# Performance work log

Measured on AMD Instinct MI355X. Metric: run time of the kernel, lower is better.

The kernel has to match this reference:

```python
import jax, jax.numpy as jnp
import numpy as np

LOG2 = 0.6931471805599453

def ssp(z):
    # SchNet shifted softplus
    return jax.nn.softplus(z) - jnp.asarray(LOG2, z.dtype)

def mlp(z, W1, b1, W2, b2):
    return ssp(z @ W1 + b1) @ W2 + b2

def _pair_idx(n_up, n_elec):
    # ordered electron pairs (i, j), i != j, grouped by spin of i and j
    n_down = n_elec - n_up
    up = np.arange(n_up)
    down = np.arange(n_up, n_elec)
    j_uu = np.stack([np.delete(up, i) for i in range(n_up)])            # [n_up, n_up-1]
    i_uu = np.repeat(up[:, None], max(n_up - 1, 0), axis=1)
    i_ud = np.repeat(up[:, None], n_down, axis=1)                        # [n_up, n_down]
    j_ud = np.broadcast_to(down, (n_up, n_down))
    i_du = np.repeat(down[:, None], n_up, axis=1)                        # [n_down, n_up]
    j_du = np.broadcast_to(up, (n_down, n_up))
    j_dd = np.stack([np.delete(down, i) for i in range(n_down)])         # [n_down, n_down-1]
    i_dd = np.repeat(down[:, None], max(n_down - 1, 0), axis=1)
    # label index: 0 = 'same', 1 = 'anti'
    return [(0, i_uu, j_uu), (1, i_ud, j_ud), (1, i_du, j_du), (0, i_dd, j_dd)]


def setup_inputs() -> dict:
    key = jax.random.key(0)
    ks = jax.random.split(key, 12)
    B, n_elec, n_nuc, dist, emb = 256, 64, 16, 32, 64
    s_in = 1.0 / np.sqrt(dist)
    s_emb = 1.0 / np.sqrt(emb)
    return {
        'x': jax.random.normal(ks[0], (B, n_elec, emb), jnp.float32),
        'Y': jax.random.normal(ks[1], (B, n_nuc, emb), jnp.float32),
        'edges_elec': jax.random.normal(ks[2], (B, n_elec, n_elec, dist), jnp.float32),
        'edges_nuc': jax.random.normal(ks[3], (B, n_elec, n_nuc, dist), jnp.float32),
        'w_W1': jax.random.normal(ks[4], (3, dist, emb), jnp.float32) * s_in,
        'w_b1': jnp.zeros((3, emb), jnp.float32),
        'w_W2': jax.random.normal(ks[5], (3, emb, emb), jnp.float32) * s_emb,
        'w_b2': jnp.zeros((3, emb), jnp.float32),
        'h_W1': jax.random.normal(ks[6], (emb, emb), jnp.float32) * s_emb,
        'h_b1': jnp.zeros((emb,), jnp.float32),
        'h_W2': jax.random.normal(ks[7], (emb, emb), jnp.float32) * s_emb,
        'h_b2': jnp.zeros((emb,), jnp.float32),
        'g_W1': jax.random.normal(ks[8], (3, emb, emb), jnp.float32) * s_emb,
        'g_b1': jnp.zeros((3, emb), jnp.float32),
        'g_W2': jax.random.normal(ks[9], (3, emb, emb), jnp.float32) * s_emb,
        'g_b2': jnp.zeros((3, emb), jnp.float32),
        'n_up': 32,
    }


def reference(x, Y, edges_elec, edges_nuc,
              w_W1, w_b1, w_W2, w_b2,
              h_W1, h_b1, h_W2, h_b2,
              g_W1, g_b1, g_W2, g_b2,
              n_up):
    n_elec = x.shape[-2]
    pairs = _pair_idx(int(n_up), n_elec)
    hx = mlp(x, h_W1, h_b1, h_W2, h_b2)  # shared h subnet, [..., n_elec, emb]
    # gather -> w subnet -> elementwise product with h(x)[j]
    msgs = [mlp(edges_elec[..., i, j, :], w_W1[l], w_b1[l], w_W2[l], w_b2[l]) * hx[..., j, :]
            for l, i, j in pairs]  # uu, ud, du, dd
    z_uu, z_ud, z_du, z_dd = (m.sum(axis=-2) for m in msgs)
    messages_el = jnp.concatenate([
        jnp.concatenate(msgs[:2], axis=-2),   # up rows: [.., n_up, n_elec-1, emb]
        jnp.concatenate(msgs[2:], axis=-2),   # down rows
    ], axis=-3)
    z_same = jnp.concatenate([z_uu, z_dd], axis=-2)
    z_anti = jnp.concatenate([z_ud, z_du], axis=-2)
    messages_nuc = mlp(edges_nuc, w_W1[2], w_b1[2], w_W2[2], w_b2[2]) * Y[..., None, :, :]
    z_nuc = messages_nuc.sum(axis=-2)
    # shared_g=False: separate g subnets (order: same, anti, n)
    update = (mlp(z_same, g_W1[0], g_b1[0], g_W2[0], g_b2[0])
              + mlp(z_anti, g_W1[1], g_b1[1], g_W2[1], g_b2[1])
              + mlp(z_nuc, g_W1[2], g_b1[2], g_W2[2], g_b2[2]))
    return update, messages_el, messages_nuc
```

## Files before the change

kernel.cpp:

```cpp
#include <hip/hip_runtime.h>
#include <hip/hip_bf16.h>

#define NE  64
#define NUP 32
#define NN  16
#define DD  32
#define EMB 64

__device__ __forceinline__ float ssp(float z) {
    float a = fabsf(z);
    float t = __expf(-a);
    return fmaxf(z, 0.0f) + __logf(1.0f + t) - 0.6931471805599453f;
}

__global__ __launch_bounds__(256) void k_hx(
    const float* __restrict__ x, const float* __restrict__ W1,
    const float* __restrict__ b1, const float* __restrict__ W2,
    const float* __restrict__ b2, float* __restrict__ hx)
{
    const int t = threadIdx.x;
    const int w = t >> 6;
    const int e = t & 63;
    const size_t row0 = (size_t)blockIdx.x * 4;

    __shared__ __align__(16) float sX[4][EMB];
    __shared__ float sh[4][EMB];

    if (t < 64) ((float4*)&sX[0][0])[t] = ((const float4*)(x + row0*EMB))[t];
    __syncthreads();

    float acc = b1[e];
    #pragma unroll
    for (int k = 0; k < EMB; ++k) acc = fmaf(sX[w][k], W1[k*EMB + e], acc);
    sh[w][e] = ssp(acc);
    __syncthreads();
    float acc2 = b2[e];
    #pragma unroll
    for (int k = 0; k < EMB; ++k) acc2 = fmaf(sh[w][k], W2[k*EMB + e], acc2);
    hx[(row0 + w)*EMB + e] = acc2;
}

__global__ __launch_bounds__(256, 3) void k_main(
    const float* __restrict__ eE,  const float* __restrict__ eN,
    const float* __restrict__ wW1, const float* __restrict__ wb1,
    const float* __restrict__ wW2, const float* __restrict__ wb2,
    const float* __restrict__ Y,   const float* __restrict__ hx,
    const float* __restrict__ gW1, const float* __restrict__ gb1,
    const float* __restrict__ gW2, const float* __restrict__ gb2,
    float* __restrict__ out_el, float* __restrict__ out_nuc, float* __restrict__ upd)
{
    const int blk = blockIdx.x;
    const int b = blk >> 6;
    const int i = blk & 63;
    const int t = threadIdx.x;
    const int w = t >> 6;
    const int e = t & 63;

    __shared__ __align__(16) float sE[NE][DD];
    __shared__ __align__(16) float sH1[NE][EMB];
    __shared__ __align__(16) float sHx[NE][EMB];
    __shared__ __align__(16) float sEN[NN][DD];
    __shared__ __align__(16) float sY[NN][EMB];
    __shared__ __align__(16) float sZp[4][EMB];
    __shared__ float sZS[EMB], sZA[EMB], sZN[EMB];
    __shared__ float sGH[3][EMB];
    __shared__ float sU[3][EMB];

    {
        const float4* eb4 = (const float4*)(eE + (size_t)blk * (NE*DD));
        float4* sE4 = (float4*)&sE[0][0];
        sE4[t]       = eb4[t];
        sE4[t + 256] = eb4[t + 256];
        const float4* hx4 = (const float4*)(hx + (size_t)b * (NE*EMB));
        float4* sHx4 = (float4*)&sHx[0][0];
        #pragma unroll
        for (int r = 0; r < 4; ++r) sHx4[t + 256*r] = hx4[t + 256*r];
        const float4* en4 = (const float4*)(eN + (size_t)blk * (NN*DD));
        if (t < 128) ((float4*)&sEN[0][0])[t] = en4[t];
        const float4* y4 = (const float4*)(Y + (size_t)b * (NN*EMB));
        ((float4*)&sY[0][0])[t] = y4[t];
    }

    const int lab_lo = (i < NUP) ? 0 : 1;
    const int lab    = (w < 2) ? lab_lo : (1 - lab_lo);

    float w1r[DD];
    #pragma unroll
    for (int k = 0; k < DD; ++k) w1r[k] = wW1[(lab*DD + k)*EMB + e];
    float w2r[EMB];
    #pragma unroll
    for (int k = 0; k < EMB; ++k) w2r[k] = wW2[(lab*EMB + k)*EMB + e];
    const float b1v = wb1[lab*EMB + e];
    const float b2v = wb2[lab*EMB + e];

    __syncthreads();

    const int j0 = w * 16;
    for (int jj = 0; jj < 16; ++jj) {
        const int j = j0 + jj;
        float acc = b1v;
        const float4* er = (const float4*)&sE[j][0];
        #pragma unroll
        for (int k4 = 0; k4 < DD/4; ++k4) {
            float4 v = er[k4];
            acc = fmaf(v.x, w1r[4*k4+0], acc);
            acc = fmaf(v.y, w1r[4*k4+1], acc);
            acc = fmaf(v.z, w1r[4*k4+2], acc);
            acc = fmaf(v.w, w1r[4*k4+3], acc);
        }
        sH1[j][e] = ssp(acc);
    }
    __syncthreads();

    float zacc = 0.0f;
    for (int jj = 0; jj < 16; ++jj) {
        const int j = j0 + jj;
        if (j == i) continue;
        float acc = b2v;
        const float4* hr = (const float4*)&sH1[j][0];
        #pragma unroll
        for (int k4 = 0; k4 < EMB/4; ++k4) {
            float4 v = hr[k4];
            acc = fmaf(v.x, w2r[4*k4+0], acc);
            acc = fmaf(v.y, w2r[4*k4+1], acc);
            acc = fmaf(v.z, w2r[4*k4+2], acc);
            acc = fmaf(v.w, w2r[4*k4+3], acc);
        }
        const float msg = acc * sHx[j][e];
        zacc += msg;
        const int p = j - (j > i ? 1 : 0);
        out_el[((size_t)blk*(NE-1) + p)*EMB + e] = msg;
    }
    sZp[w][e] = zacc;

    #pragma unroll
    for (int k = 0; k < DD; ++k) w1r[k] = wW1[(2*DD + k)*EMB + e];
    #pragma unroll
    for (int k = 0; k < EMB; ++k) w2r[k] = wW2[(2*EMB + k)*EMB + e];
    const float b1n = wb1[2*EMB + e];
    const float b2n = wb2[2*EMB + e];

    __syncthreads();

    if (t < 128) {
        const int which = w;
        const bool take_lo = ((which == 0) == (lab_lo == 0));
        const float v = take_lo ? (sZp[0][e] + sZp[1][e]) : (sZp[2][e] + sZp[3][e]);
        float* dst = (which == 0) ? sZS : sZA;
        dst[e] = v;
    }

    const int n0 = w * 4;
    for (int nn = 0; nn < 4; ++nn) {
        const int n = n0 + nn;
        float acc = b1n;
        const float4* er = (const float4*)&sEN[n][0];
        #pragma unroll
        for (int k4 = 0; k4 < DD/4; ++k4) {
            float4 v = er[k4];
            acc = fmaf(v.x, w1r[4*k4+0], acc);
            acc = fmaf(v.y, w1r[4*k4+1], acc);
            acc = fmaf(v.z, w1r[4*k4+2], acc);
            acc = fmaf(v.w, w1r[4*k4+3], acc);
        }
        sH1[n][e] = ssp(acc);
    }
    __syncthreads();

    float zn = 0.0f;
    for (int nn = 0; nn < 4; ++nn) {
        const int n = n0 + nn;
        float acc = b2n;
        const float4* hr = (const float4*)&sH1[n][0];
        #pragma unroll
        for (int k4 = 0; k4 < EMB/4; ++k4) {
            float4 v = hr[k4];
            acc = fmaf(v.x, w2r[4*k4+0], acc);
            acc = fmaf(v.y, w2r[4*k4+1], acc);
            acc = fmaf(v.z, w2r[4*k4+2], acc);
            acc = fmaf(v.w, w2r[4*k4+3], acc);
        }
        const float msg = acc * sY[n][e];
        zn += msg;
        out_nuc[((size_t)blk*NN + n)*EMB + e] = msg;
    }
    sZp[w][e] = zn;
    __syncthreads();
    if (t < 64) sZN[e] = sZp[0][e] + sZp[1][e] + sZp[2][e] + sZp[3][e];
    __syncthreads();

    if (w < 3) {
        const float* z = (w == 0) ? sZS : (w == 1) ? sZA : sZN;
        float acc = gb1[w*EMB + e];
        #pragma unroll
        for (int k = 0; k < EMB; ++k) acc = fmaf(z[k], gW1[(w*EMB + k)*EMB + e], acc);
        sGH[w][e] = ssp(acc);
    }
    __syncthreads();
    if (w < 3) {
        float acc2 = gb2[w*EMB + e];
        #pragma unroll
        for (int k = 0; k < EMB; ++k) acc2 = fmaf(sGH[w][k], gW2[(w*EMB + k)*EMB + e], acc2);
        sU[w][e] = acc2;
    }
    __syncthreads();
    if (t < 64) upd[(size_t)blk*EMB + e] = sU[0][e] + sU[1][e] + sU[2][e];
}

extern "C" void kernel_launch(void* const* d_in, const int* in_sizes, int n_in,
                              void* d_out, int out_size, void* d_ws, size_t ws_size,
                              hipStream_t stream)
{
    const float* x   = (const float*)d_in[0];
    const float* Y   = (const float*)d_in[1];
    const float* eE  = (const float*)d_in[2];
    const float* eN  = (const float*)d_in[3];
    const float* wW1 = (const float*)d_in[4];
    const float* wb1 = (const float*)d_in[5];
    const float* wW2 = (const float*)d_in[6];
    const float* wb2 = (const float*)d_in[7];
    const float* hW1 = (const float*)d_in[8];
    const float* hb1 = (const float*)d_in[9];
    const float* hW2 = (const float*)d_in[10];
    const float* hb2 = (const float*)d_in[11];
    const float* gW1 = (const float*)d_in[12];
    const float* gb1 = (const float*)d_in[13];
    const float* gW2 = (const float*)d_in[14];
    const float* gb2 = (const float*)d_in[15];

    const int B   = in_sizes[0] / (NE * EMB);
    const int nbi = B * NE;

    float* hx = (float*)d_ws;

    float* upd     = (float*)d_out;
    float* out_el  = upd    + (size_t)nbi * EMB;
    float* out_nuc = out_el + (size_t)nbi * (NE-1) * EMB;

    k_hx  <<<nbi/4, 256, 0, stream>>>(x, hW1, hb1, hW2, hb2, hx);
    k_main<<<nbi,   256, 0, stream>>>(eE, eN, wW1, wb1, wW2, wb2, Y, hx,
                                      gW1, gb1, gW2, gb2, out_el, out_nuc, upd);
}
```

Before: 819.3 us.

## Move edge and h-subnet MLPs onto bf16x3 split MFMA with prepacked weight fragments

Replaces the scalar FMA per-thread matvec loops for the w- and h-subnet MLPs with 16x16x32 bf16 MFMA instructions. Each fp32 operand is split into hi and lo bf16 parts and three MFMAs are issued to keep accuracy close to fp32. A new pre-kernel splits and packs the weights into per-lane fragment order in workspace. Edge tiles are loaded straight into registers instead of staged through LDS. This aims to cut the ALU-bound FMA cost and the register pressure from holding 96 weights per thread. It adds split/convert overhead and an extra launch, and carries some precision risk.

```diff
diff --git a/kernel.cpp b/kernel.cpp
--- a/kernel.cpp
+++ b/kernel.cpp
@@ -7,204 +7,310 @@
 #define DD  32
 #define EMB 64
 
+typedef __attribute__((ext_vector_type(8))) short bf16x8;
+typedef __attribute__((ext_vector_type(4))) float f32x4;
+
+#define W1H_OFF  0
+#define W1L_OFF  6144
+#define W2H_OFF  12288
+#define W2L_OFF  24576
+#define HW1H_OFF 36864
+#define HW1L_OFF 40960
+#define HW2H_OFF 45056
+#define HW2L_OFF 49152
+
 __device__ __forceinline__ float ssp(float z) {
     float a = fabsf(z);
     float t = __expf(-a);
     return fmaxf(z, 0.0f) + __logf(1.0f + t) - 0.6931471805599453f;
 }
 
+__device__ __forceinline__ void split1(float x, unsigned short& hi, unsigned short& lo) {
+    unsigned u = __float_as_uint(x);
+    hi = (unsigned short)(u >> 16);
+    float r = x - __uint_as_float(u & 0xFFFF0000u);
+    lo = (unsigned short)(__float_as_uint(r) >> 16);
+}
+
+__device__ __forceinline__ void split8(const float* v, bf16x8& hi, bf16x8& lo) {
+    #pragma unroll
+    for (int j = 0; j < 8; ++j) {
+        unsigned u = __float_as_uint(v[j]);
+        hi[j] = (short)(u >> 16);
+        float r = v[j] - __uint_as_float(u & 0xFFFF0000u);
+        lo[j] = (short)(__float_as_uint(r) >> 16);
+    }
+}
+
+__device__ __forceinline__ bf16x8 ldfrag(const unsigned short* p) {
+    return *(const bf16x8*)p;
+}
+
+#define MFMA3(acc, ah, al, bh, bl)                                            \
+    acc = __builtin_amdgcn_mfma_f32_16x16x32_bf16(al, bh, acc, 0, 0, 0);      \
+    acc = __builtin_amdgcn_mfma_f32_16x16x32_bf16(ah, bl, acc, 0, 0, 0);      \
+    acc = __builtin_amdgcn_mfma_f32_16x16x32_bf16(ah, bh, acc, 0, 0, 0);
+
+__global__ __launch_bounds__(256) void k_wsplit(
+    const float* __restrict__ wW1, const float* __restrict__ wW2,
+    const float* __restrict__ hW1, const float* __restrict__ hW2,
+    unsigned short* __restrict__ fr)
+{
+    const int idx = blockIdx.x * 256 + threadIdx.x;
+    if (idx < 6144) {
+        int j = idx & 7, l = (idx >> 3) & 63, nt = (idx >> 9) & 3, lab = idx >> 11;
+        int k = (l >> 4) * 8 + j, n = nt * 16 + (l & 15);
+        unsigned short h, lo2; split1(wW1[lab*DD*EMB + k*EMB + n], h, lo2);
+        fr[W1H_OFF + idx] = h; fr[W1L_OFF + idx] = lo2;
+    }
+    if (idx < 12288) {
+        int j = idx & 7, l = (idx >> 3) & 63, kc = (idx >> 9) & 1, nt = (idx >> 10) & 3, lab = idx >> 12;
+        int k = kc*32 + (l >> 4)*8 + j, n = nt*16 + (l & 15);
+        unsigned short h, lo2; split1(wW2[lab*EMB*EMB + k*EMB + n], h, lo2);
+        fr[W2H_OFF + idx] = h; fr[W2L_OFF + idx] = lo2;
+    }
+    if (idx < 4096) {
+        int j = idx & 7, l = (idx >> 3) & 63, kc = (idx >> 9) & 1, nt = idx >> 10;
+        int k = kc*32 + (l >> 4)*8 + j, n = nt*16 + (l & 15);
+        unsigned short h, lo2;
+        split1(hW1[k*EMB + n], h, lo2);
+        fr[HW1H_OFF + idx] = h; fr[HW1L_OFF + idx] = lo2;
+        split1(hW2[k*EMB + n], h, lo2);
+        fr[HW2H_OFF + idx] = h; fr[HW2L_OFF + idx] = lo2;
+    }
+}
+
 __global__ __launch_bounds__(256) void k_hx(
-    const float* __restrict__ x, const float* __restrict__ W1,
-    const float* __restrict__ b1, const float* __restrict__ W2,
-    const float* __restrict__ b2, float* __restrict__ hx)
+    const float* __restrict__ x, const float* __restrict__ hb1,
+    const float* __restrict__ hb2, const unsigned short* __restrict__ fr,
+    float* __restrict__ hx)
 {
     const int t = threadIdx.x;
-    const int w = t >> 6;
-    const int e = t & 63;
-    const size_t row0 = (size_t)blockIdx.x * 4;
-
-    __shared__ __align__(16) float sX[4][EMB];
-    __shared__ float sh[4][EMB];
-
-    if (t < 64) ((float4*)&sX[0][0])[t] = ((const float4*)(x + row0*EMB))[t];
-    __syncthreads();
-
-    float acc = b1[e];
-    #pragma unroll
-    for (int k = 0; k < EMB; ++k) acc = fmaf(sX[w][k], W1[k*EMB + e], acc);
-    sh[w][e] = ssp(acc);
-    __syncthreads();
-    float acc2 = b2[e];
-    #pragma unroll
-    for (int k = 0; k < EMB; ++k) acc2 = fmaf(sh[w][k], W2[k*EMB + e], acc2);
-    hx[(row0 + w)*EMB + e] = acc2;
+    const int w = t >> 6, lane = t & 63;
+    const int lrow = lane & 15, g = lane >> 4, lk8 = g * 8;
+    const size_t base = (size_t)blockIdx.x * 64;
+
+    __shared__ __align__(16) unsigned short sH1h[64*72], sH1l[64*72];
+
+    bf16x8 ah[2], al[2];
+    #pragma unroll
+    for (int kc = 0; kc < 2; ++kc) {
+        float v[8];
+        const float* xr = x + (base + 16*w + lrow) * EMB + kc*32 + lk8;
+        *(float4*)v = *(const float4*)xr; *(float4*)(v+4) = *(const float4*)(xr+4);
+        split8(v, ah[kc], al[kc]);
+    }
+    #pragma unroll
+    for (int nt = 0; nt < 4; ++nt) {
+        f32x4 acc = {0.f,0.f,0.f,0.f};
+        #pragma unroll
+        for (int kc = 0; kc < 2; ++kc) {
+            bf16x8 bh = ldfrag(fr + HW1H_OFF + ((nt*2 + kc)*64 + lane)*8);
+            bf16x8 bl = ldfrag(fr + HW1L_OFF + ((nt*2 + kc)*64 + lane)*8);
+            MFMA3(acc, ah[kc], al[kc], bh, bl);
+        }
+        const float b1v = hb1[nt*16 + lrow];
+        #pragma unroll
+        for (int r = 0; r < 4; ++r) {
+            float h = ssp(acc[r] + b1v);
+            unsigned short hi, lo; split1(h, hi, lo);
+            const int row = 16*w + g*4 + r, col = nt*16 + lrow;
+            sH1h[row*72 + col] = hi; sH1l[row*72 + col] = lo;
+        }
+    }
+    __syncthreads();
+    #pragma unroll
+    for (int kc = 0; kc < 2; ++kc) {
+        const int off = (16*w + lrow)*72 + kc*32 + lk8;
+        ah[kc] = *(const bf16x8*)&sH1h[off];
+        al[kc] = *(const bf16x8*)&sH1l[off];
+    }
+    #pragma unroll
+    for (int nt = 0; nt < 4; ++nt) {
+        f32x4 acc = {0.f,0.f,0.f,0.f};
+        #pragma unroll
+        for (int kc = 0; kc < 2; ++kc) {
+            bf16x8 bh = ldfrag(fr + HW2H_OFF + ((nt*2 + kc)*64 + lane)*8);
+            bf16x8 bl = ldfrag(fr + HW2L_OFF + ((nt*2 + kc)*64 + lane)*8);
+            MFMA3(acc, ah[kc], al[kc], bh, bl);
+        }
+        const float b2v = hb2[nt*16 + lrow];
+        #pragma unroll
+        for (int r = 0; r < 4; ++r) {
+            const size_t grow = base + 16*w + g*4 + r;
+            hx[grow*EMB + nt*16 + lrow] = acc[r] + b2v;
+        }
+    }
 }
 
 __global__ __launch_bounds__(256, 3) void k_main(
     const float* __restrict__ eE,  const float* __restrict__ eN,
-    const float* __restrict__ wW1, const float* __restrict__ wb1,
-    const float* __restrict__ wW2, const float* __restrict__ wb2,
+    const float* __restrict__ wb1, const float* __restrict__ wb2,
     const float* __restrict__ Y,   const float* __restrict__ hx,
     const float* __restrict__ gW1, const float* __restrict__ gb1,
     const float* __restrict__ gW2, const float* __restrict__ gb2,
+    const unsigned short* __restrict__ fr,
     float* __restrict__ out_el, float* __restrict__ out_nuc, float* __restrict__ upd)
 {
     const int blk = blockIdx.x;
-    const int b = blk >> 6;
-    const int i = blk & 63;
+    const int b = blk >> 6, i = blk & 63;
     const int t = threadIdx.x;
-    const int w = t >> 6;
-    const int e = t & 63;
-
-    __shared__ __align__(16) float sE[NE][DD];
-    __shared__ __align__(16) float sH1[NE][EMB];
-    __shared__ __align__(16) float sHx[NE][EMB];
-    __shared__ __align__(16) float sEN[NN][DD];
-    __shared__ __align__(16) float sY[NN][EMB];
-    __shared__ __align__(16) float sZp[4][EMB];
+    const int w = t >> 6, lane = t & 63;
+    const int lrow = lane & 15, g = lane >> 4, lk8 = g * 8;
+
+    __shared__ __align__(16) unsigned short sH1h[64*72], sH1l[64*72];
+    __shared__ __align__(16) float sHx[NE*EMB];
+    __shared__ __align__(16) float sY[NN*EMB];
+    __shared__ float sZw[4][EMB];
     __shared__ float sZS[EMB], sZA[EMB], sZN[EMB];
-    __shared__ float sGH[3][EMB];
-    __shared__ float sU[3][EMB];
-
-    {
-        const float4* eb4 = (const float4*)(eE + (size_t)blk * (NE*DD));
-        float4* sE4 = (float4*)&sE[0][0];
-        sE4[t]       = eb4[t];
-        sE4[t + 256] = eb4[t + 256];
+    __shared__ float sGH[3][EMB], sU[3][EMB];
+
+    {
         const float4* hx4 = (const float4*)(hx + (size_t)b * (NE*EMB));
-        float4* sHx4 = (float4*)&sHx[0][0];
-        #pragma unroll
-        for (int r = 0; r < 4; ++r) sHx4[t + 256*r] = hx4[t + 256*r];
-        const float4* en4 = (const float4*)(eN + (size_t)blk * (NN*DD));
-        if (t < 128) ((float4*)&sEN[0][0])[t] = en4[t];
-        const float4* y4 = (const float4*)(Y + (size_t)b * (NN*EMB));
-        ((float4*)&sY[0][0])[t] = y4[t];
+        float4* d4 = (float4*)sHx;
+        #pragma unroll
+        for (int r = 0; r < 4; ++r) d4[t + 256*r] = hx4[t + 256*r];
+        ((float4*)sY)[t] = ((const float4*)(Y + (size_t)b * (NN*EMB)))[t];
     }
 
     const int lab_lo = (i < NUP) ? 0 : 1;
-    const int lab    = (w < 2) ? lab_lo : (1 - lab_lo);
-
-    float w1r[DD];
-    #pragma unroll
-    for (int k = 0; k < DD; ++k) w1r[k] = wW1[(lab*DD + k)*EMB + e];
-    float w2r[EMB];
-    #pragma unroll
-    for (int k = 0; k < EMB; ++k) w2r[k] = wW2[(lab*EMB + k)*EMB + e];
-    const float b1v = wb1[lab*EMB + e];
-    const float b2v = wb2[lab*EMB + e];
-
-    __syncthreads();
-
-    const int j0 = w * 16;
-    for (int jj = 0; jj < 16; ++jj) {
-        const int j = j0 + jj;
-        float acc = b1v;
-        const float4* er = (const float4*)&sE[j][0];
-        #pragma unroll
-        for (int k4 = 0; k4 < DD/4; ++k4) {
-            float4 v = er[k4];
-            acc = fmaf(v.x, w1r[4*k4+0], acc);
-            acc = fmaf(v.y, w1r[4*k4+1], acc);
-            acc = fmaf(v.z, w1r[4*k4+2], acc);
-            acc = fmaf(v.w, w1r[4*k4+3], acc);
-        }
-        sH1[j][e] = ssp(acc);
-    }
-    __syncthreads();
-
-    float zacc = 0.0f;
-    for (int jj = 0; jj < 16; ++jj) {
-        const int j = j0 + jj;
-        if (j == i) continue;
-        float acc = b2v;
-        const float4* hr = (const float4*)&sH1[j][0];
-        #pragma unroll
-        for (int k4 = 0; k4 < EMB/4; ++k4) {
-            float4 v = hr[k4];
-            acc = fmaf(v.x, w2r[4*k4+0], acc);
-            acc = fmaf(v.y, w2r[4*k4+1], acc);
-            acc = fmaf(v.z, w2r[4*k4+2], acc);
-            acc = fmaf(v.w, w2r[4*k4+3], acc);
-        }
-        const float msg = acc * sHx[j][e];
-        zacc += msg;
-        const int p = j - (j > i ? 1 : 0);
-        out_el[((size_t)blk*(NE-1) + p)*EMB + e] = msg;
-    }
-    sZp[w][e] = zacc;
-
-    #pragma unroll
-    for (int k = 0; k < DD; ++k) w1r[k] = wW1[(2*DD + k)*EMB + e];
-    #pragma unroll
-    for (int k = 0; k < EMB; ++k) w2r[k] = wW2[(2*EMB + k)*EMB + e];
-    const float b1n = wb1[2*EMB + e];
-    const float b2n = wb2[2*EMB + e];
-
+    const int lab = ((w < 2) == (i < NUP)) ? 0 : 1;
+
+    {
+        float v[8];
+        const float* er = eE + (size_t)blk*(NE*DD) + (16*w + lrow)*DD + lk8;
+        *(float4*)v = *(const float4*)er; *(float4*)(v+4) = *(const float4*)(er+4);
+        bf16x8 eh, el; split8(v, eh, el);
+        #pragma unroll
+        for (int nt = 0; nt < 4; ++nt) {
+            bf16x8 bh = ldfrag(fr + W1H_OFF + ((lab*4 + nt)*64 + lane)*8);
+            bf16x8 bl = ldfrag(fr + W1L_OFF + ((lab*4 + nt)*64 + lane)*8);
+            f32x4 acc = {0.f,0.f,0.f,0.f};
+            MFMA3(acc, eh, el, bh, bl);
+            const float b1v = wb1[lab*EMB + nt*16 + lrow];
+            #pragma unroll
+            for (int r = 0; r < 4; ++r) {
+                float h = ssp(acc[r] + b1v);
+                unsigned short hi, lo; split1(h, hi, lo);
+                const int row = 16*w + g*4 + r, col = nt*16 + lrow;
+                sH1h[row*72 + col] = hi; sH1l[row*72 + col] = lo;
+            }
+        }
+    }
+    __syncthreads();
+
+    {
+        bf16x8 ah[2], al[2];
+        #pragma unroll
+        for (int kc = 0; kc < 2; ++kc) {
+            const int off = (16*w + lrow)*72 + kc*32 + lk8;
+            ah[kc] = *(const bf16x8*)&sH1h[off];
+            al[kc] = *(const bf16x8*)&sH1l[off];
+        }
+        #pragma unroll
+        for (int nt = 0; nt < 4; ++nt) {
+            f32x4 acc = {0.f,0.f,0.f,0.f};
+            #pragma unroll
+            for (int kc = 0; kc < 2; ++kc) {
+                bf16x8 bh = ldfrag(fr + W2H_OFF + (((lab*4 + nt)*2 + kc)*64 + lane)*8);
+                bf16x8 bl = ldfrag(fr + W2L_OFF + (((lab*4 + nt)*2 + kc)*64 + lane)*8);
+                MFMA3(acc, ah[kc], al[kc], bh, bl);
+            }
+            const float bv = wb2[lab*EMB + nt*16 + lrow];
+            float zp = 0.f;
+            #pragma unroll
+            for (int r = 0; r < 4; ++r) {
+                const int j = 16*w + g*4 + r;
+                const int e = nt*16 + lrow;
+                const float msg = (acc[r] + bv) * sHx[j*EMB + e];
+                if (j != i) {
+                    zp += msg;
+                    out_el[((size_t)blk*(NE-1) + (j - (j > i ? 1 : 0)))*EMB + e] = msg;
+                }
+            }
+            zp += __shfl_xor(zp, 16);
+            zp += __shfl_xor(zp, 32);
+            if (lane < 16) sZw[w][nt*16 + lane] = zp;
+        }
+    }
+    __syncthreads();
+
+    {
+        float v[8];
+        const float* er = eN + (size_t)blk*(NN*DD) + lrow*DD + lk8;
+        *(float4*)v = *(const float4*)er; *(float4*)(v+4) = *(const float4*)(er+4);
+        bf16x8 eh, el; split8(v, eh, el);
+        bf16x8 bh = ldfrag(fr + W1H_OFF + ((2*4 + w)*64 + lane)*8);
+        bf16x8 bl = ldfrag(fr + W1L_OFF + ((2*4 + w)*64 + lane)*8);
+        f32x4 acc = {0.f,0.f,0.f,0.f};
+        MFMA3(acc, eh, el, bh, bl);
+        const float b1n = wb1[2*EMB + w*16 + lrow];
+        #pragma unroll
+        for (int r = 0; r < 4; ++r) {
+            float h = ssp(acc[r] + b1n);
+            unsigned short hi, lo; split1(h, hi, lo);
+            const int row = g*4 + r, col = w*16 + lrow;
+            sH1h[row*72 + col] = hi; sH1l[row*72 + col] = lo;
+        }
+    }
+    __syncthreads();
+
+    {
+        bf16x8 ah[2], al[2];
+        #pragma unroll
+        for (int kc = 0; kc < 2; ++kc) {
+            const int off = lrow*72 + kc*32 + lk8;
+            ah[kc] = *(const bf16x8*)&sH1h[off];
+            al[kc] = *(const bf16x8*)&sH1l[off];
+        }
+        f32x4 acc = {0.f,0.f,0.f,0.f};
+        #pragma unroll
+        for (int kc = 0; kc < 2; ++kc) {
+            bf16x8 bh = ldfrag(fr + W2H_OFF + (((2*4 + w)*2 + kc)*64 + lane)*8);
+            bf16x8 bl = ldfrag(fr + W2L_OFF + (((2*4 + w)*2 + kc)*64 + lane)*8);
+            MFMA3(acc, ah[kc], al[kc], bh, bl);
+        }
+        const float b2n = wb2[2*EMB + w*16 + lrow];
+        float zp = 0.f;
+        #pragma unroll
+        for (int r = 0; r < 4; ++r) {
+            const int nrow = g*4 + r;
+            const int e = w*16 + lrow;
+            const float m = (acc[r] + b2n) * sY[nrow*EMB + e];
+            zp += m;
+            out_nuc[((size_t)blk*NN + nrow)*EMB + e] = m;
+        }
+        zp += __shfl_xor(zp, 16);
+        zp += __shfl_xor(zp, 32);
+        if (lane < 16) sZN[w*16 + lane] = zp;
+    }
     __syncthreads();
 
     if (t < 128) {
         const int which = w;
+        const int e2 = t & 63;
         const bool take_lo = ((which == 0) == (lab_lo == 0));
-        const float v = take_lo ? (sZp[0][e] + sZp[1][e]) : (sZp[2][e] + sZp[3][e]);
-        float* dst = (which == 0) ? sZS : sZA;
-        dst[e] = v;
-    }
-
-    const int n0 = w * 4;
-    for (int nn = 0; nn < 4; ++nn) {
-        const int n = n0 + nn;
-        float acc = b1n;
-        const float4* er = (const float4*)&sEN[n][0];
-        #pragma unroll
-        for (int k4 = 0; k4 < DD/4; ++k4) {
-            float4 v = er[k4];
-            acc = fmaf(v.x, w1r[4*k4+0], acc);
-            acc = fmaf(v.y, w1r[4*k4+1], acc);
-            acc = fmaf(v.z, w1r[4*k4+2], acc);
-            acc = fmaf(v.w, w1r[4*k4+3], acc);
-        }
-        sH1[n][e] = ssp(acc);
-    }
-    __syncthreads();
-
-    float zn = 0.0f;
-    for (int nn = 0; nn < 4; ++nn) {
-        const int n = n0 + nn;
-        float acc = b2n;
-        const float4* hr = (const float4*)&sH1[n][0];
-        #pragma unroll
-        for (int k4 = 0; k4 < EMB/4; ++k4) {
-            float4 v = hr[k4];
-            acc = fmaf(v.x, w2r[4*k4+0], acc);
-            acc = fmaf(v.y, w2r[4*k4+1], acc);
-            acc = fmaf(v.z, w2r[4*k4+2], acc);
-            acc = fmaf(v.w, w2r[4*k4+3], acc);
-        }
-        const float msg = acc * sY[n][e];
-        zn += msg;
-        out_nuc[((size_t)blk*NN + n)*EMB + e] = msg;
-    }
-    sZp[w][e] = zn;
-    __syncthreads();
-    if (t < 64) sZN[e] = sZp[0][e] + sZp[1][e] + sZp[2][e] + sZp[3][e];
+        const float v = take_lo ? (sZw[0][e2] + sZw[1][e2]) : (sZw[2][e2] + sZw[3][e2]);
+        (which == 0 ? sZS : sZA)[e2] = v;
+    }
     __syncthreads();
 
     if (w < 3) {
         const float* z = (w == 0) ? sZS : (w == 1) ? sZA : sZN;
-        float acc = gb1[w*EMB + e];
-        #pragma unroll
-        for (int k = 0; k < EMB; ++k) acc = fmaf(z[k], gW1[(w*EMB + k)*EMB + e], acc);
-        sGH[w][e] = ssp(acc);
+        float acc = gb1[w*EMB + lane];
+        #pragma unroll
+        for (int k = 0; k < EMB; ++k) acc = fmaf(z[k], gW1[(w*EMB + k)*EMB + lane], acc);
+        sGH[w][lane] = ssp(acc);
     }
     __syncthreads();
     if (w < 3) {
-        float acc2 = gb2[w*EMB + e];
-        #pragma unroll
-        for (int k = 0; k < EMB; ++k) acc2 = fmaf(sGH[w][k], gW2[(w*EMB + k)*EMB + e], acc2);
-        sU[w][e] = acc2;
-    }
-    __syncthreads();
-    if (t < 64) upd[(size_t)blk*EMB + e] = sU[0][e] + sU[1][e] + sU[2][e];
+        float acc2 = gb2[w*EMB + lane];
+        #pragma unroll
+        for (int k = 0; k < EMB; ++k) acc2 = fmaf(sGH[w][k], gW2[(w*EMB + k)*EMB + lane], acc2);
+        sU[w][lane] = acc2;
+    }
+    __syncthreads();
+    if (t < 64) upd[(size_t)blk*EMB + t] = sU[0][t] + sU[1][t] + sU[2][t];
 }
 
 extern "C" void kernel_launch(void* const* d_in, const int* in_sizes, int n_in,
@@ -232,12 +338,15 @@
     const int nbi = B * NE;
 
     float* hx = (float*)d_ws;
+    unsigned short* fr = (unsigned short*)((char*)d_ws + (size_t)nbi*EMB*4);
 
     float* upd     = (float*)d_out;
     float* out_el  = upd    + (size_t)nbi * EMB;
     float* out_nuc = out_el + (size_t)nbi * (NE-1) * EMB;
 
-    k_hx  <<<nbi/4, 256, 0, stream>>>(x, hW1, hb1, hW2, hb2, hx);
-    k_main<<<nbi,   256, 0, stream>>>(eE, eN, wW1, wb1, wW2, wb2, Y, hx,
-                                      gW1, gb1, gW2, gb2, out_el, out_nuc, upd);
-}
+    k_wsplit<<<48,     256, 0, stream>>>(wW1, wW2, hW1, hW2, fr);
+    k_hx    <<<nbi/64, 256, 0, stream>>>(x, hb1, hb2, fr, hx);
+    k_main  <<<nbi,    256, 0, stream>>>(eE, eN, wb1, wb2, Y, hx,
+                                         gW1, gb1, gW2, gb2, fr,
+                                         out_el, out_nuc, upd);
+}
```

Result: faster. 676.3 us (-17.5%).
